# Kernel tuning notes

Hardware: AMD Instinct MI355X
Metric: run time of the kernel (lower is better)

Reference implementation:

```python
import jax, jax.numpy as jnp
import numpy as np

NUM_NODES = 100000
NUM_EDGES = 600000
NUM_GRAPHS = 512
D = 128  # num_features == latent widths


def setup_inputs() -> dict:
    key = jax.random.key(0)
    ks = jax.random.split(key, 16)
    inp = {
        "x": jax.random.normal(ks[0], (NUM_NODES, D), dtype=jnp.float32),
        "edge_index": jax.random.randint(ks[1], (2, NUM_EDGES), 0, NUM_NODES, dtype=jnp.int32),
        "batch": jnp.sort(jax.random.randint(ks[2], (NUM_NODES,), 0, NUM_GRAPHS, dtype=jnp.int32)),
    }
    s = 1.0 / np.sqrt(D)
    # SAGEConv params per layer: lin_l (applied to mean-aggregated neighbors), lin_r (root), bias
    for i in range(3):
        inp[f"Wl{i+1}"] = jax.random.uniform(ks[3 + 3 * i], (D, D), jnp.float32, -s, s)
        inp[f"Wr{i+1}"] = jax.random.uniform(ks[4 + 3 * i], (D, D), jnp.float32, -s, s)
        inp[f"b{i+1}"] = jax.random.uniform(ks[5 + 3 * i], (D,), jnp.float32, -s, s)
    inp["Wro"] = jax.random.uniform(ks[12], (D, 1), jnp.float32, -s, s)
    inp["bro"] = jax.random.uniform(ks[13], (1,), jnp.float32, -s, s)
    return inp


def _sage_conv(h, Wl, Wr, b, src, dst):
    # mean aggregation of source features at destination nodes
    msg = jax.ops.segment_sum(h[src], dst, num_segments=NUM_NODES)          # [N, D]
    cnt = jax.ops.segment_sum(jnp.ones((src.shape[0], 1), h.dtype), dst,
                              num_segments=NUM_NODES)                        # [N, 1]
    mean = msg / jnp.maximum(cnt, 1.0)
    return mean @ Wl + h @ Wr + b


def reference(x, edge_index, batch, Wl1, Wr1, b1, Wl2, Wr2, b2, Wl3, Wr3, b3, Wro, bro):
    src, dst = edge_index[0], edge_index[1]
    h = x
    for Wl, Wr, b in ((Wl1, Wr1, b1), (Wl2, Wr2, b2), (Wl3, Wr3, b3)):
        h = jax.nn.relu(_sage_conv(h, Wl, Wr, b, src, dst))
    # per-graph sum pooling (replaces the python loop over unique batch ids)
    pooled = jax.ops.segment_sum(h, batch, num_segments=NUM_GRAPHS)  # [G, D]
    return jax.nn.sigmoid(pooled @ Wro + bro)  # [G, 1]
```

## Files before the change

### kernel.cpp

```cpp
#include <hip/hip_runtime.h>
#include <math.h>

#define N_NODES 100000
#define N_EDGES 600000
#define N_GRAPHS 512
#define D 128
#define SCAN_BS 1024
#define SCAN_NBC ((N_NODES + SCAN_BS - 1) / SCAN_BS)

typedef unsigned short u16;
typedef __attribute__((ext_vector_type(8))) short short8;
typedef __attribute__((ext_vector_type(4))) float f32x4;

__device__ __forceinline__ u16 f2bf(float f) {
    unsigned int u = __float_as_uint(f);
    u += 0x7FFFu + ((u >> 16) & 1u);
    return (u16)(u >> 16);
}
__device__ __forceinline__ float bf2f(u16 h) {
    return __uint_as_float(((unsigned int)h) << 16);
}
__device__ __forceinline__ void split2(float f, unsigned int& h16, unsigned int& l16) {
    unsigned int u = __float_as_uint(f);
    unsigned int hb = (u + (0x7FFFu + ((u >> 16) & 1u))) & 0xffff0000u;
    float lo = f - __uint_as_float(hb);
    unsigned int ul = __float_as_uint(lo);
    h16 = hb >> 16;
    l16 = (ul + (0x7FFFu + ((ul >> 16) & 1u))) >> 16;
}

__global__ __launch_bounds__(256) void zero_i_kernel(int* __restrict__ p, int n) {
    int i = blockIdx.x * 256 + threadIdx.x;
    if (i < n) p[i] = 0;
}

__global__ __launch_bounds__(256) void hist_kernel(const int* __restrict__ dst,
                                                   int* __restrict__ deg) {
    int e = blockIdx.x * 256 + threadIdx.x;
    if (e < N_EDGES) atomicAdd(&deg[dst[e]], 1);
}

__global__ __launch_bounds__(1024) void scan1_kernel(const int* __restrict__ deg,
                                                     int* __restrict__ excl,
                                                     int* __restrict__ blocksum) {
    __shared__ int buf[2][SCAN_BS];
    const int t = threadIdx.x;
    const int gid = blockIdx.x * SCAN_BS + t;
    int v = (gid < N_NODES) ? deg[gid] : 0;
    buf[0][t] = v;
    __syncthreads();
    int pi = 0;
    for (int off = 1; off < SCAN_BS; off <<= 1) {
        int val = buf[pi][t];
        if (t >= off) val += buf[pi][t - off];
        buf[pi ^ 1][t] = val;
        pi ^= 1;
        __syncthreads();
    }
    int incl = buf[pi][t];
    if (gid < N_NODES) excl[gid] = incl - v;
    if (t == SCAN_BS - 1) blocksum[blockIdx.x] = incl;
}

__global__ __launch_bounds__(256) void scan3_kernel(const int* __restrict__ excl,
                                                    const int* __restrict__ blocksum,
                                                    int* __restrict__ rowptr) {
    __shared__ int buf[2][128];
    const int t = threadIdx.x;
    if (t < 128) buf[0][t] = (t < SCAN_NBC) ? blocksum[t] : 0;
    __syncthreads();
    int pi = 0;
    for (int off = 1; off < 128; off <<= 1) {
        if (t < 128) {
            int val = buf[pi][t];
            if (t >= off) val += buf[pi][t - off];
            buf[pi ^ 1][t] = val;
        }
        pi ^= 1;
        __syncthreads();
    }
    const int i = blockIdx.x * 256 + t;
    if (i < N_NODES) {
        const int j = i / SCAN_BS;
        const int pref = (j == 0) ? 0 : buf[pi][j - 1];
        rowptr[i] = excl[i] + pref;
    }
    if (i == 0) rowptr[N_NODES] = N_EDGES;
}

__global__ __launch_bounds__(256) void fill_kernel(const int* __restrict__ src,
                                                   const int* __restrict__ dst,
                                                   const int* __restrict__ rowptr,
                                                   int* __restrict__ fill,
                                                   int* __restrict__ csr_src) {
    int e = blockIdx.x * 256 + threadIdx.x;
    if (e < N_EDGES) {
        int d = dst[e];
        int pos = rowptr[d] + atomicAdd(&fill[d], 1);
        csr_src[pos] = src[e];
    }
}

__global__ __launch_bounds__(256) void split_x_kernel(const float* __restrict__ x,
                                                      u16* __restrict__ Hhi,
                                                      u16* __restrict__ Hlo) {
    const int i = blockIdx.x * 256 + threadIdx.x;
    const float4 v = ((const float4*)x)[i];
    unsigned int h0, l0, h1, l1, h2, l2, h3, l3;
    split2(v.x, h0, l0); split2(v.y, h1, l1);
    split2(v.z, h2, l2); split2(v.w, h3, l3);
    uint2 oh, ol;
    oh.x = h0 | (h1 << 16); oh.y = h2 | (h3 << 16);
    ol.x = l0 | (l1 << 16); ol.y = l2 | (l3 << 16);
    ((uint2*)Hhi)[i] = oh;
    ((uint2*)Hlo)[i] = ol;
}

__global__ __launch_bounds__(64) void wprep_kernel(const float* __restrict__ Wl1, const float* __restrict__ Wr1,
                                                   const float* __restrict__ Wl2, const float* __restrict__ Wr2,
                                                   const float* __restrict__ Wl3, const float* __restrict__ Wr3,
                                                   u16* __restrict__ wph, u16* __restrict__ wpl) {
    const int layer = blockIdx.x >> 6;
    const int t = blockIdx.x & 63;
    const int lane = threadIdx.x;
    const float* Wl = (layer == 0) ? Wl1 : (layer == 1) ? Wl2 : Wl3;
    const float* Wr = (layer == 0) ? Wr1 : (layer == 1) ? Wr2 : Wr3;
    const int nt = t >> 3, kt = t & 7;
    const int n = nt * 16 + (lane & 15);
    const int k0 = kt * 32 + (lane >> 4) * 8;
    const size_t base = (size_t)layer * 32768 + (size_t)(t * 64 + lane) * 8;
    #pragma unroll
    for (int j = 0; j < 8; ++j) {
        const int k = k0 + j;
        const float w = (k < 128) ? Wl[k * 128 + n] : Wr[(k - 128) * 128 + n];
        const u16 h = f2bf(w);
        wph[base + j] = h;
        wpl[base + j] = f2bf(w - bf2f(h));
    }
}

__global__ __launch_bounds__(256) void agg_kernel(const u16* __restrict__ Hhi,
                                                  const int* __restrict__ rowptr,
                                                  const int* __restrict__ csr_src,
                                                  u16* __restrict__ Mb) {
    const int lane = threadIdx.x & 63;
    const int node = blockIdx.x * 4 + (threadIdx.x >> 6);
    if (node >= N_NODES) return;
    const int beg = rowptr[node];
    const int end = rowptr[node + 1];
    const unsigned int* H32 = (const unsigned int*)Hhi;
    float a0 = 0.f, a1 = 0.f;

    for (int c0 = beg; c0 < end; c0 += 64) {
        const int nv = min(64, end - c0);
        int msrc = (c0 + lane < end) ? csr_src[c0 + lane] : 0;
        int j = 0;
        for (; j + 4 <= nv; j += 4) {
            const int s0 = __shfl(msrc, j + 0);
            const int s1 = __shfl(msrc, j + 1);
            const int s2 = __shfl(msrc, j + 2);
            const int s3 = __shfl(msrc, j + 3);
            const unsigned int w0 = H32[(size_t)s0 * 64 + lane];
            const unsigned int w1 = H32[(size_t)s1 * 64 + lane];
            const unsigned int w2 = H32[(size_t)s2 * 64 + lane];
            const unsigned int w3 = H32[(size_t)s3 * 64 + lane];
            a0 += __uint_as_float(w0 << 16) + __uint_as_float(w1 << 16)
                + __uint_as_float(w2 << 16) + __uint_as_float(w3 << 16);
            a1 += __uint_as_float(w0 & 0xffff0000u) + __uint_as_float(w1 & 0xffff0000u)
                + __uint_as_float(w2 & 0xffff0000u) + __uint_as_float(w3 & 0xffff0000u);
        }
        for (; j < nv; ++j) {
            const int s = __shfl(msrc, j);
            const unsigned int w = H32[(size_t)s * 64 + lane];
            a0 += __uint_as_float(w << 16);
            a1 += __uint_as_float(w & 0xffff0000u);
        }
    }
    const float inv = 1.0f / (float)max(end - beg, 1);
    const unsigned int o = (unsigned int)f2bf(a0 * inv) | ((unsigned int)f2bf(a1 * inv) << 16);
    ((unsigned int*)Mb)[(size_t)node * 64 + lane] = o;
}

__global__ __launch_bounds__(512, 4) void gemm_kernel(const u16* __restrict__ Mb,
                                                      const u16* Hhi, const u16* Hlo,
                                                      const u16* __restrict__ Wph,
                                                      const u16* __restrict__ Wpl,
                                                      const float* __restrict__ bias,
                                                      u16* OHhi, u16* OHlo,
                                                      const float* __restrict__ Wro,
                                                      float* rowdot) {
    __shared__ uint4 ldsW[4096];
    const int t = threadIdx.x;
    const int lane = t & 63;
    const int wv = t >> 6;
    const int m0 = blockIdx.x * 128 + wv * 16;
    int rm = m0 + (lane & 15);
    if (rm >= N_NODES) rm = 0;
    const int ko = (lane >> 4) * 8;

    short8 am[4], ah[4], al[4];
    #pragma unroll
    for (int kt = 0; kt < 4; ++kt) {
        am[kt] = *(const short8*)(Mb  + (size_t)rm * D + kt * 32 + ko);
        ah[kt] = *(const short8*)(Hhi + (size_t)rm * D + kt * 32 + ko);
        al[kt] = *(const short8*)(Hlo + (size_t)rm * D + kt * 32 + ko);
    }

    const int rowb = m0 + ((lane >> 4) << 2);
    const int cl = lane & 15;
    const u16* ldsU = (const u16*)ldsW;
    float wsum[4] = {0.f, 0.f, 0.f, 0.f};

    #pragma unroll
    for (int s = 0; s < 2; ++s) {
        if (s) __syncthreads();
        {
            const uint4* gh = (const uint4*)Wph + s * 2048;
            const uint4* gl = (const uint4*)Wpl + s * 2048;
            #pragma unroll
            for (int i = 0; i < 4; ++i) {
                ldsW[t + 512 * i]        = gh[t + 512 * i];
                ldsW[2048 + t + 512 * i] = gl[t + 512 * i];
            }
        }
        __syncthreads();

        #pragma unroll
        for (int nt2 = 0; nt2 < 4; ++nt2) {
            f32x4 acc = {0.f, 0.f, 0.f, 0.f};
            #pragma unroll
            for (int kt = 0; kt < 8; ++kt) {
                const int fo = (nt2 * 8 + kt) * 512 + lane * 8;
                const short8 bh = *(const short8*)(ldsU + fo);
                const short8 bl = *(const short8*)(ldsU + 16384 + fo);
                if (kt < 4) {
                    acc = __builtin_amdgcn_mfma_f32_16x16x32_bf16(am[kt], bh, acc, 0, 0, 0);
                    acc = __builtin_amdgcn_mfma_f32_16x16x32_bf16(am[kt], bl, acc, 0, 0, 0);
                } else {
                    acc = __builtin_amdgcn_mfma_f32_16x16x32_bf16(ah[kt - 4], bh, acc, 0, 0, 0);
                    acc = __builtin_amdgcn_mfma_f32_16x16x32_bf16(ah[kt - 4], bl, acc, 0, 0, 0);
                    acc = __builtin_amdgcn_mfma_f32_16x16x32_bf16(al[kt - 4], bh, acc, 0, 0, 0);
                }
            }
            const int col = (s * 4 + nt2) * 16 + cl;
            const float bv = bias[col];
            const float wroc = rowdot ? Wro[col] : 0.f;
            #pragma unroll
            for (int r = 0; r < 4; ++r) {
                const int row = rowb + r;
                const float v = fmaxf(acc[r] + bv, 0.f);
                if (rowdot) {
                    wsum[r] = fmaf(v, wroc, wsum[r]);
                } else if (row < N_NODES) {
                    unsigned int h16, l16;
                    split2(v, h16, l16);
                    OHhi[(size_t)row * D + col] = (u16)h16;
                    OHlo[(size_t)row * D + col] = (u16)l16;
                }
            }
        }
    }

    if (rowdot) {
        #pragma unroll
        for (int r = 0; r < 4; ++r) {
            float tsum = wsum[r];
            tsum += __shfl_down(tsum, 8, 64);
            tsum += __shfl_down(tsum, 4, 64);
            tsum += __shfl_down(tsum, 2, 64);
            tsum += __shfl_down(tsum, 1, 64);
            const int row = rowb + r;
            if (cl == 0 && row < N_NODES) {
                rowdot[row] = tsum;
            }
        }
    }
}

__global__ __launch_bounds__(64) void final_kernel(const float* __restrict__ rowdot,
                                                   const int* __restrict__ batch,
                                                   const float* __restrict__ bro,
                                                   float* __restrict__ out) {
    const int g = blockIdx.x;
    const int t = threadIdx.x;
    int lo = 0, hi = N_NODES;
    while (lo < hi) { int mid = (lo + hi) >> 1; if (batch[mid] < g) lo = mid + 1; else hi = mid; }
    int lo2 = lo, hi2 = N_NODES;
    while (lo2 < hi2) { int mid = (lo2 + hi2) >> 1; if (batch[mid] < g + 1) lo2 = mid + 1; else hi2 = mid; }

    float acc = 0.0f;
    for (int i = lo + t; i < lo2; i += 64) acc += rowdot[i];
    #pragma unroll
    for (int off = 32; off > 0; off >>= 1) acc += __shfl_down(acc, off, 64);
    if (t == 0) out[g] = 1.0f / (1.0f + expf(-(acc + bro[0])));
}

extern "C" void kernel_launch(void* const* d_in, const int* in_sizes, int n_in,
                              void* d_out, int out_size, void* d_ws, size_t ws_size,
                              hipStream_t stream) {
    const float* x     = (const float*)d_in[0];
    const int*   ei    = (const int*)d_in[1];
    const int*   batch = (const int*)d_in[2];
    const int*   src   = ei;
    const int*   dst   = ei + N_EDGES;
    const float* Wl[3] = {(const float*)d_in[3], (const float*)d_in[6], (const float*)d_in[9]};
    const float* Wr[3] = {(const float*)d_in[4], (const float*)d_in[7], (const float*)d_in[10]};
    const float* bs[3] = {(const float*)d_in[5], (const float*)d_in[8], (const float*)d_in[11]};
    const float* Wro   = (const float*)d_in[12];
    const float* bro   = (const float*)d_in[13];
    float* out = (float*)d_out;

    const size_t ND = (size_t)N_NODES * D;
    char* ws = (char*)d_ws;
    u16* Hhi = (u16*)ws;
    u16* Hlo = Hhi + ND;
    u16* Mb  = Hlo + ND;
    u16* Wph = Mb + ND;
    u16* Wpl = Wph + 3 * 32768;
    int* deg      = (int*)(Wpl + 3 * 32768);
    int* fill     = deg + N_NODES;
    float* rowdot = (float*)(fill + N_NODES);
    int* excl     = (int*)(rowdot + N_NODES);
    int* blocksum = excl + N_NODES;
    int* rowptr   = blocksum + 128;
    int* csr_src  = rowptr + N_NODES + 1;

    const int EB      = (N_EDGES + 255) / 256;
    const int NB      = (N_NODES + 255) / 256;
    const int NB2     = (2 * N_NODES + 255) / 256;
    const int SPLIT_B = (int)(ND / 4 / 256);
    const int AGG_B   = N_NODES / 4;
    const int GEMM_B  = (N_NODES + 127) / 128;

    zero_i_kernel<<<NB2, 256, 0, stream>>>(deg, 2 * N_NODES);
    hist_kernel<<<EB, 256, 0, stream>>>(dst, deg);
    scan1_kernel<<<SCAN_NBC, SCAN_BS, 0, stream>>>(deg, excl, blocksum);
    scan3_kernel<<<NB, 256, 0, stream>>>(excl, blocksum, rowptr);
    fill_kernel<<<EB, 256, 0, stream>>>(src, dst, rowptr, fill, csr_src);

    split_x_kernel<<<SPLIT_B, 256, 0, stream>>>(x, Hhi, Hlo);
    wprep_kernel<<<192, 64, 0, stream>>>(Wl[0], Wr[0], Wl[1], Wr[1], Wl[2], Wr[2], Wph, Wpl);

    for (int l = 0; l < 3; ++l) {
        float* rdl = (l == 2) ? rowdot : (float*)nullptr;
        agg_kernel<<<AGG_B, 256, 0, stream>>>(Hhi, rowptr, csr_src, Mb);
        gemm_kernel<<<GEMM_B, 512, 0, stream>>>(Mb, Hhi, Hlo,
                                                Wph + l * 32768, Wpl + l * 32768, bs[l],
                                                Hhi, Hlo, Wro, rdl);
    }

    final_kernel<<<N_GRAPHS, 64, 0, stream>>>(rowdot, batch, bro, out);
}
```

Before: 404.1 us.

## Stage GEMM weights via direct global-to-LDS loads and coalesce output stores through LDS

Weight tiles are now copied into LDS with global_load_lds instructions, so the data no longer passes through VGPRs. The epilogue that wrote scattered 2-byte hi/lo outputs now stages each wave's 16x64 tile in a per-wave, XOR-swizzled LDS bounce buffer and writes it out as 16-byte coalesced rows. This targets the poor store coalescing and the register cost of staging the weights. In exchange it uses more LDS (80KB per block), which may limit occupancy, and it adds extra LDS traffic with manual waitcnt barriers.

```diff
diff --git a/kernel.cpp b/kernel.cpp
--- a/kernel.cpp
+++ b/kernel.cpp
@@ -27,6 +27,12 @@
     unsigned int ul = __float_as_uint(lo);
     h16 = hb >> 16;
     l16 = (ul + (0x7FFFu + ((ul >> 16) & 1u))) >> 16;
+}
+
+typedef __attribute__((address_space(1))) const unsigned int gas_u32;
+typedef __attribute__((address_space(3))) unsigned int las_u32;
+__device__ __forceinline__ void gload16(const void* g, void* l) {
+    __builtin_amdgcn_global_load_lds((gas_u32*)g, (las_u32*)l, 16, 0, 0);
 }
 
 __global__ __launch_bounds__(256) void zero_i_kernel(int* __restrict__ p, int n) {
@@ -189,7 +195,7 @@
                                                       u16* OHhi, u16* OHlo,
                                                       const float* __restrict__ Wro,
                                                       float* rowdot) {
-    __shared__ uint4 ldsW[4096];
+    __shared__ uint4 ldsAll[5120];
     const int t = threadIdx.x;
     const int lane = t & 63;
     const int wv = t >> 6;
@@ -208,7 +214,9 @@
 
     const int rowb = m0 + ((lane >> 4) << 2);
     const int cl = lane & 15;
-    const u16* ldsU = (const u16*)ldsW;
+    const int g4 = (lane >> 4) << 2;
+    const u16* ldsU = (const u16*)ldsAll;
+    char* bounceB = (char*)ldsAll + 65536 + wv * 2048;
     float wsum[4] = {0.f, 0.f, 0.f, 0.f};
 
     #pragma unroll
@@ -219,12 +227,13 @@
             const uint4* gl = (const uint4*)Wpl + s * 2048;
             #pragma unroll
             for (int i = 0; i < 4; ++i) {
-                ldsW[t + 512 * i]        = gh[t + 512 * i];
-                ldsW[2048 + t + 512 * i] = gl[t + 512 * i];
+                gload16(gh + t + 512 * i, (void*)&ldsAll[wv * 64 + 512 * i]);
+                gload16(gl + t + 512 * i, (void*)&ldsAll[2048 + wv * 64 + 512 * i]);
             }
         }
         __syncthreads();
 
+        f32x4 acc4[4];
         #pragma unroll
         for (int nt2 = 0; nt2 < 4; ++nt2) {
             f32x4 acc = {0.f, 0.f, 0.f, 0.f};
@@ -242,21 +251,69 @@
                     acc = __builtin_amdgcn_mfma_f32_16x16x32_bf16(al[kt - 4], bh, acc, 0, 0, 0);
                 }
             }
-            const int col = (s * 4 + nt2) * 16 + cl;
-            const float bv = bias[col];
-            const float wroc = rowdot ? Wro[col] : 0.f;
-            #pragma unroll
-            for (int r = 0; r < 4; ++r) {
-                const int row = rowb + r;
-                const float v = fmaxf(acc[r] + bv, 0.f);
-                if (rowdot) {
+            acc4[nt2] = acc;
+        }
+
+        if (rowdot) {
+            #pragma unroll
+            for (int nt2 = 0; nt2 < 4; ++nt2) {
+                const int col = (s * 4 + nt2) * 16 + cl;
+                const float bv = bias[col];
+                const float wroc = Wro[col];
+                #pragma unroll
+                for (int r = 0; r < 4; ++r) {
+                    const float v = fmaxf(acc4[nt2][r] + bv, 0.f);
                     wsum[r] = fmaf(v, wroc, wsum[r]);
-                } else if (row < N_NODES) {
+                }
+            }
+        } else {
+            unsigned int lo_pack[8];
+            #pragma unroll
+            for (int nt2 = 0; nt2 < 4; ++nt2) {
+                const int col = (s * 4 + nt2) * 16 + cl;
+                const float bv = bias[col];
+                #pragma unroll
+                for (int r = 0; r < 4; ++r) {
+                    const int row16 = g4 + r;
+                    const float v = fmaxf(acc4[nt2][r] + bv, 0.f);
                     unsigned int h16, l16;
                     split2(v, h16, l16);
-                    OHhi[(size_t)row * D + col] = (u16)h16;
-                    OHlo[(size_t)row * D + col] = (u16)l16;
+                    const int boff = (row16 * 128 + (nt2 * 16 + cl) * 2) ^ ((row16 & 7) << 4);
+                    *(u16*)(bounceB + boff) = (u16)h16;
+                    if (r & 1) lo_pack[nt2 * 2 + (r >> 1)] |= l16 << 16;
+                    else       lo_pack[nt2 * 2 + (r >> 1)]  = l16;
                 }
+            }
+            asm volatile("s_waitcnt lgkmcnt(0)" ::: "memory");
+            #pragma unroll
+            for (int j = 0; j < 2; ++j) {
+                const int row16 = j * 8 + (lane >> 3);
+                const int blk = lane & 7;
+                const uint4 vv = *(const uint4*)(bounceB + row16 * 128 + ((blk ^ (row16 & 7)) << 4));
+                const int grow = blockIdx.x * 128 + wv * 16 + row16;
+                if (grow < N_NODES)
+                    *(uint4*)(OHhi + (size_t)grow * D + s * 64 + blk * 8) = vv;
+            }
+            asm volatile("s_waitcnt lgkmcnt(0)" ::: "memory");
+            #pragma unroll
+            for (int nt2 = 0; nt2 < 4; ++nt2) {
+                #pragma unroll
+                for (int r = 0; r < 4; ++r) {
+                    const int row16 = g4 + r;
+                    const unsigned int l16 = (lo_pack[nt2 * 2 + (r >> 1)] >> ((r & 1) * 16)) & 0xffffu;
+                    const int boff = (row16 * 128 + (nt2 * 16 + cl) * 2) ^ ((row16 & 7) << 4);
+                    *(u16*)(bounceB + boff) = (u16)l16;
+                }
+            }
+            asm volatile("s_waitcnt lgkmcnt(0)" ::: "memory");
+            #pragma unroll
+            for (int j = 0; j < 2; ++j) {
+                const int row16 = j * 8 + (lane >> 3);
+                const int blk = lane & 7;
+                const uint4 vv = *(const uint4*)(bounceB + row16 * 128 + ((blk ^ (row16 & 7)) << 4));
+                const int grow = blockIdx.x * 128 + wv * 16 + row16;
+                if (grow < N_NODES)
+                    *(uint4*)(OHlo + (size_t)grow * D + s * 64 + blk * 8) = vv;
             }
         }
     }
```

New measurement: 406.3 us. Within noise of the previous version (+0.6%).
